# Kernel optimization log

Measured on AMD Instinct MI355X. Metric: run time of the kernel, lower is better.

## Reference

```python
import jax, jax.numpy as jnp
import numpy as np

N_NODES = 100000

def gcn_conv(x, edge_index, W, b):
    # PyG GCNConv: y = D^{-1/2} (A + I) D^{-1/2} X W + b
    N = x.shape[0]
    xw = x @ W  # transform first (smaller feature dim for message passing)
    loop = jnp.arange(N, dtype=edge_index.dtype)
    src = jnp.concatenate([edge_index[0], loop])
    dst = jnp.concatenate([edge_index[1], loop])
    ones = jnp.ones(dst.shape[0], dtype=xw.dtype)
    deg = jax.ops.segment_sum(ones, dst, num_segments=N)
    dinv = jnp.where(deg > 0, jax.lax.rsqrt(deg), 0.0)
    norm = dinv[src] * dinv[dst]  # [E+N]
    msg = xw[src] * norm[:, None]  # gather + scale
    out = jax.ops.segment_sum(msg, dst, num_segments=N)  # scatter-add
    return out + b

def setup_inputs() -> dict:
    key = jax.random.key(0)
    k1, k2, k3, k4, k5 = jax.random.split(key, 5)
    num_features, hidden, num_classes = 500, 64, 40
    x = jax.random.normal(k1, (N_NODES, num_features), dtype=jnp.float32)
    edge_index = jax.random.randint(k2, (2, 1600000), 0, N_NODES, dtype=jnp.int64)
    # Glorot-style init for GCNConv weights, zero bias (PyG default)
    W1 = jax.random.normal(k3, (num_features, hidden), dtype=jnp.float32) / np.sqrt(num_features)
    b1 = jnp.zeros((hidden,), dtype=jnp.float32)
    W2 = jax.random.normal(k4, (hidden, num_classes), dtype=jnp.float32) / np.sqrt(hidden)
    b2 = jnp.zeros((num_classes,), dtype=jnp.float32)
    return {"x": x, "edge_index": edge_index, "W1": W1, "b1": b1, "W2": W2, "b2": b2}

def reference(x, edge_index, W1, b1, W2, b2):
    h = gcn_conv(x, edge_index, W1, b1)
    h = jax.nn.relu(h)
    # dropout is identity in eval mode (training=False)
    logits = gcn_conv(h, edge_index, W2, b2)
    return (jax.nn.log_softmax(logits, axis=1), logits)
```

## Files before the change

kernel.cpp:

```cpp
#include <hip/hip_runtime.h>
#include <hip/hip_bf16.h>
#include <math.h>

#define N_NODES 100000
#define F_IN    500
#define HID     64
#define NCLS    40
#define NBKT    ((N_NODES + 255) / 256)
#define CAP     8192

typedef __attribute__((ext_vector_type(8))) short short8v;
typedef __attribute__((ext_vector_type(4))) float floatx4;
typedef unsigned short ushort_t;
typedef unsigned int uint_t;

__device__ __forceinline__ float bflo(uint_t u) {
    union { uint_t i; float f; } v; v.i = u << 16; return v.f;
}
__device__ __forceinline__ float bfhi(uint_t u) {
    union { uint_t i; float f; } v; v.i = u & 0xffff0000u; return v.f;
}
__device__ __forceinline__ ushort_t f2bf(float f) {
    __hip_bfloat16 b = __float2bfloat16(f);
    return *(ushort_t*)&b;
}
__device__ __forceinline__ uint_t pack2(float a, float b) {
    return (uint_t)f2bf(a) | ((uint_t)f2bf(b) << 16);
}

__global__ __launch_bounds__(256) void prep_kernel(const float* __restrict__ W1,
                                                   ushort_t* __restrict__ W1T,
                                                   int* __restrict__ bcursor) {
    if (blockIdx.x == 0) {
        bcursor[threadIdx.x]       = threadIdx.x * CAP;
        bcursor[threadIdx.x + 256] = (threadIdx.x + 256) * CAP;
    }
    int idx = blockIdx.x * 256 + threadIdx.x;
    if (idx >= HID * 512) return;
    int nn = idx >> 9;
    int k  = idx & 511;
    float v = (k < F_IN) ? W1[(size_t)k * HID + nn] : 0.0f;
    W1T[idx] = f2bf(v);
}

__global__ __launch_bounds__(512) void fill_kernel(const int* __restrict__ src,
                                                   const int* __restrict__ dst,
                                                   int* __restrict__ bcursor,
                                                   int* __restrict__ pairs, int E) {
    __shared__ int c[NBKT];
    __shared__ int base[NBKT];
    for (int i = threadIdx.x; i < NBKT; i += 512) c[i] = 0;
    __syncthreads();
    int chunk = (E + gridDim.x - 1) / gridDim.x;
    int lo = blockIdx.x * chunk;
    int hi = min(lo + chunk, E);
    for (int e = lo + threadIdx.x; e < hi; e += 512) atomicAdd(&c[dst[e] >> 8], 1);
    __syncthreads();
    for (int i = threadIdx.x; i < NBKT; i += 512) {
        int nn = c[i];
        base[i] = nn ? atomicAdd(&bcursor[i], nn) : 0;
    }
    __syncthreads();
    for (int i = threadIdx.x; i < NBKT; i += 512) c[i] = 0;
    __syncthreads();
    for (int e = lo + threadIdx.x; e < hi; e += 512) {
        int d = dst[e];
        int b = d >> 8;
        int p = base[b] + atomicAdd(&c[b], 1);
        if (p < (b + 1) * CAP) pairs[p] = src[e] | ((d & 255) << 17);
    }
}

__global__ __launch_bounds__(256) void b_fine_kernel(const int* __restrict__ pairs,
                                                     const int* __restrict__ bcursor,
                                                     int2* __restrict__ rse,
                                                     int* __restrict__ col,
                                                     float* __restrict__ dinv, int n) {
    __shared__ int w[CAP];
    __shared__ int cs[CAP];
    __shared__ int cnt[256];
    __shared__ int scn[256];
    __shared__ int cur[256];
    int b = blockIdx.x;
    int nb0 = b << 8;
    int nodes = min(256, n - nb0);
    int g0 = b * CAP;
    int size = min(bcursor[b] - g0, CAP);
    int tid = threadIdx.x;

    for (int i = tid; i < size; i += 256) w[i] = pairs[g0 + i];
    cnt[tid] = 0;
    __syncthreads();
    for (int i = tid; i < size; i += 256) atomicAdd(&cnt[w[i] >> 17], 1);
    __syncthreads();
    int v = cnt[tid];
    scn[tid] = v;
    __syncthreads();
    for (int off = 1; off < 256; off <<= 1) {
        int t = (tid >= off) ? scn[tid - off] : 0;
        __syncthreads();
        scn[tid] += t;
        __syncthreads();
    }
    int excl = scn[tid] - v;
    cur[tid] = excl;
    if (tid < nodes) {
        rse[nb0 + tid] = make_int2(g0 + excl, g0 + excl + v);
        dinv[nb0 + tid] = rsqrtf((float)(v + 1));
    }
    __syncthreads();
    for (int i = tid; i < size; i += 256) {
        int word = w[i];
        int lpos = atomicAdd(&cur[word >> 17], 1);
        cs[lpos] = word & 0x1FFFF;
    }
    __syncthreads();
    for (int i = tid; i < size; i += 256) col[g0 + i] = cs[i];
}

__global__ __launch_bounds__(256) void gemm1_mfma(const float* __restrict__ x,
                                                  const ushort_t* __restrict__ W1T,
                                                  const float* __restrict__ dinv,
                                                  ushort_t* __restrict__ xws, int n) {
    __shared__ __align__(16) ushort_t As[2][128 * 72];
    const int tid  = threadIdx.x;
    const int wave = tid >> 6;
    const int lane = tid & 63;
    const int m16  = lane & 15;
    const int q    = lane >> 4;
    const int r0   = blockIdx.x * 128;

    floatx4 acc[2][4];
#pragma unroll
    for (int i = 0; i < 2; i++)
#pragma unroll
        for (int j = 0; j < 4; j++) acc[i][j] = (floatx4){0.f, 0.f, 0.f, 0.f};

    const int kg    = tid & 15;
    const int rbase = tid >> 4;

    floatx4 pf[8];
    const floatx4 zero4 = (floatx4){0.f, 0.f, 0.f, 0.f};
    {
        const int k4 = kg * 4;
#pragma unroll
        for (int rr = 0; rr < 8; rr++) {
            int gr = r0 + rbase + rr * 16;
            pf[rr] = (gr < n) ? __builtin_nontemporal_load((const floatx4*)&x[(size_t)gr * F_IN + k4])
                              : zero4;
        }
#pragma unroll
        for (int rr = 0; rr < 8; rr++) {
            int row = rbase + rr * 16;
            *(uint2*)&As[0][row * 72 + kg * 4] =
                make_uint2(pack2(pf[rr][0], pf[rr][1]), pack2(pf[rr][2], pf[rr][3]));
        }
    }
    __syncthreads();

    for (int it = 0; it < 8; it++) {
        const int cur = it & 1;
        if (it < 7) {
            const int k4 = (it + 1) * 64 + kg * 4;
            const bool kok = (k4 < F_IN);
#pragma unroll
            for (int rr = 0; rr < 8; rr++) {
                int gr = r0 + rbase + rr * 16;
                pf[rr] = (kok && gr < n)
                           ? __builtin_nontemporal_load((const floatx4*)&x[(size_t)gr * F_IN + k4])
                           : zero4;
            }
        }
        const int kb = it * 64;
#pragma unroll
        for (int kt = 0; kt < 2; kt++) {
            const int ko = kt * 32 + q * 8;
            short8v a0 = *(const short8v*)&As[cur][(wave * 32 + m16) * 72 + ko];
            short8v a1 = *(const short8v*)&As[cur][(wave * 32 + 16 + m16) * 72 + ko];
#pragma unroll
            for (int nt = 0; nt < 4; nt++) {
                short8v b = *(const short8v*)&W1T[(size_t)(nt * 16 + m16) * 512 + kb + ko];
                acc[0][nt] = __builtin_amdgcn_mfma_f32_16x16x32_bf16(a0, b, acc[0][nt], 0, 0, 0);
                acc[1][nt] = __builtin_amdgcn_mfma_f32_16x16x32_bf16(a1, b, acc[1][nt], 0, 0, 0);
            }
        }
        if (it < 7) {
#pragma unroll
            for (int rr = 0; rr < 8; rr++) {
                int row = rbase + rr * 16;
                *(uint2*)&As[1 - cur][row * 72 + kg * 4] =
                    make_uint2(pack2(pf[rr][0], pf[rr][1]), pack2(pf[rr][2], pf[rr][3]));
            }
            __syncthreads();
        }
    }

#pragma unroll
    for (int mt = 0; mt < 2; mt++) {
#pragma unroll
        for (int i = 0; i < 4; i++) {
            int gr = r0 + wave * 32 + mt * 16 + q * 4 + i;
            if (gr < n) {
                float di = dinv[gr];
#pragma unroll
                for (int nt = 0; nt < 4; nt++) {
                    xws[(size_t)gr * HID + nt * 16 + m16] = f2bf(acc[mt][nt][i] * di);
                }
            }
        }
    }
}

__global__ __launch_bounds__(256) void agg1_kernel(const ushort_t* __restrict__ xws,
                                                   const int* __restrict__ col,
                                                   const int2* __restrict__ rse,
                                                   const float* __restrict__ dinv,
                                                   const float* __restrict__ b1,
                                                   ushort_t* __restrict__ hs, int n) {
    int d = blockIdx.x * 4 + (threadIdx.x >> 6);
    if (d >= n) return;
    int lane = threadIdx.x & 63;
    int g = lane >> 3;
    int c = lane & 7;
    int2 se = rse[d];
    int start = se.x, end = se.y;
    uint4 selfv = *(const uint4*)&xws[(size_t)d * HID + c * 8];
    float acc[8];
#pragma unroll
    for (int i = 0; i < 8; i++) acc[i] = 0.f;
    for (int j = start; j < end; j += 32) {
#pragma unroll
        for (int t = 0; t < 4; t++) {
            int e = j + t * 8 + g;
            if (e < end) {
                int s = col[e];
                uint4 v = *(const uint4*)&xws[(size_t)s * HID + c * 8];
                acc[0] += bflo(v.x); acc[1] += bfhi(v.x);
                acc[2] += bflo(v.y); acc[3] += bfhi(v.y);
                acc[4] += bflo(v.z); acc[5] += bfhi(v.z);
                acc[6] += bflo(v.w); acc[7] += bfhi(v.w);
            }
        }
    }
#pragma unroll
    for (int off = 8; off <= 32; off <<= 1) {
#pragma unroll
        for (int i = 0; i < 8; i++) acc[i] += __shfl_xor(acc[i], off);
    }
    acc[0] += bflo(selfv.x); acc[1] += bfhi(selfv.x);
    acc[2] += bflo(selfv.y); acc[3] += bfhi(selfv.y);
    acc[4] += bflo(selfv.z); acc[5] += bfhi(selfv.z);
    acc[6] += bflo(selfv.w); acc[7] += bfhi(selfv.w);
    if (g == 0) {
        float di = dinv[d];
        float4 b0 = *(const float4*)&b1[c * 8];
        float4 b4 = *(const float4*)&b1[c * 8 + 4];
        uint4 o;
        o.x = pack2(fmaxf(di * acc[0] + b0.x, 0.f) * di, fmaxf(di * acc[1] + b0.y, 0.f) * di);
        o.y = pack2(fmaxf(di * acc[2] + b0.z, 0.f) * di, fmaxf(di * acc[3] + b0.w, 0.f) * di);
        o.z = pack2(fmaxf(di * acc[4] + b4.x, 0.f) * di, fmaxf(di * acc[5] + b4.y, 0.f) * di);
        o.w = pack2(fmaxf(di * acc[6] + b4.z, 0.f) * di, fmaxf(di * acc[7] + b4.w, 0.f) * di);
        *(uint4*)&hs[(size_t)d * HID + c * 8] = o;
    }
}

__global__ __launch_bounds__(256) void agg2_lsm_kernel(const ushort_t* __restrict__ hs,
                                                       const int* __restrict__ col,
                                                       const int2* __restrict__ rse,
                                                       const float* __restrict__ dinv,
                                                       const float* __restrict__ W2,
                                                       const float* __restrict__ b2,
                                                       float* __restrict__ out, int n) {
    __shared__ float W2L[HID * 41];
    for (int i = threadIdx.x; i < HID * NCLS; i += 256) {
        int j = i / NCLS, k = i % NCLS;
        W2L[j * 41 + k] = W2[i];
    }
    __syncthreads();

    int d = blockIdx.x * 4 + (threadIdx.x >> 6);
    if (d >= n) return;
    int lane = threadIdx.x & 63;
    int g = lane >> 3;
    int c = lane & 7;
    int2 se = rse[d];
    int start = se.x, end = se.y;
    uint4 selfv = *(const uint4*)&hs[(size_t)d * HID + c * 8];
    float acc[8];
#pragma unroll
    for (int i = 0; i < 8; i++) acc[i] = 0.f;
    for (int j = start; j < end; j += 32) {
#pragma unroll
        for (int t = 0; t < 4; t++) {
            int e = j + t * 8 + g;
            if (e < end) {
                int s = col[e];
                uint4 v = *(const uint4*)&hs[(size_t)s * HID + c * 8];
                acc[0] += bflo(v.x); acc[1] += bfhi(v.x);
                acc[2] += bflo(v.y); acc[3] += bfhi(v.y);
                acc[4] += bflo(v.z); acc[5] += bfhi(v.z);
                acc[6] += bflo(v.w); acc[7] += bfhi(v.w);
            }
        }
    }
#pragma unroll
    for (int off = 8; off <= 32; off <<= 1) {
#pragma unroll
        for (int i = 0; i < 8; i++) acc[i] += __shfl_xor(acc[i], off);
    }
    acc[0] += bflo(selfv.x); acc[1] += bfhi(selfv.x);
    acc[2] += bflo(selfv.y); acc[3] += bfhi(selfv.y);
    acc[4] += bflo(selfv.z); acc[5] += bfhi(selfv.z);
    acc[6] += bflo(selfv.w); acc[7] += bfhi(selfv.w);

    float o[5];
#pragma unroll
    for (int kk = 0; kk < 5; kk++) {
        float s = 0.f;
#pragma unroll
        for (int i = 0; i < 8; i++)
            s += acc[i] * W2L[(c * 8 + i) * 41 + g * 5 + kk];
        o[kk] = s;
    }
#pragma unroll
    for (int off = 1; off < 8; off <<= 1) {
#pragma unroll
        for (int kk = 0; kk < 5; kk++) o[kk] += __shfl_xor(o[kk], off);
    }

    float di = dinv[d];
    float v[5];
#pragma unroll
    for (int kk = 0; kk < 5; kk++) v[kk] = di * o[kk] + b2[g * 5 + kk];

    float m = fmaxf(fmaxf(fmaxf(v[0], v[1]), fmaxf(v[2], v[3])), v[4]);
#pragma unroll
    for (int off = 8; off <= 32; off <<= 1) m = fmaxf(m, __shfl_xor(m, off));
    float s = __expf(v[0] - m) + __expf(v[1] - m) + __expf(v[2] - m)
            + __expf(v[3] - m) + __expf(v[4] - m);
#pragma unroll
    for (int off = 8; off <= 32; off <<= 1) s += __shfl_xor(s, off);

    if (c == 0) {
        float lg = __logf(s);
        float* lsm    = out;
        float* logits = out + (size_t)N_NODES * NCLS;
        size_t base = (size_t)d * NCLS + g * 5;
#pragma unroll
        for (int kk = 0; kk < 5; kk++) {
            logits[base + kk] = v[kk];
            lsm[base + kk]    = v[kk] - m - lg;
        }
    }
}

extern "C" void kernel_launch(void* const* d_in, const int* in_sizes, int n_in,
                              void* d_out, int out_size, void* d_ws, size_t ws_size,
                              hipStream_t stream) {
    const float* x  = (const float*)d_in[0];
    const int*   ei = (const int*)d_in[1];
    const float* W1 = (const float*)d_in[2];
    const float* b1 = (const float*)d_in[3];
    const float* W2 = (const float*)d_in[4];
    const float* b2 = (const float*)d_in[5];

    const int N = N_NODES;
    const int E = in_sizes[1] / 2;
    const int* src = ei;
    const int* dst = ei + E;

    ushort_t* xws  = (ushort_t*)d_ws;
    ushort_t* hsb  = xws + (size_t)N * HID;
    ushort_t* W1T  = hsb + (size_t)N * HID;
    float* dinv    = (float*)(W1T + (size_t)HID * 512);
    int2*  rse     = (int2*)(dinv + N);
    int*   bcursor = (int*)(rse + N);
    int*   pairs   = bcursor + 512;
    int*   col     = pairs + (size_t)NBKT * CAP;

    const int NB_W = (N + 3) / 4;

    prep_kernel<<<(HID * 512 + 255) / 256, 256, 0, stream>>>(W1, W1T, bcursor);

    fill_kernel<<<256, 512, 0, stream>>>(src, dst, bcursor, pairs, E);

    b_fine_kernel<<<NBKT, 256, 0, stream>>>(pairs, bcursor, rse, col, dinv, N);

    gemm1_mfma<<<(N + 127) / 128, 256, 0, stream>>>(x, W1T, dinv, xws, N);

    agg1_kernel<<<NB_W, 256, 0, stream>>>(xws, col, rse, dinv, b1, hsb, N);

    agg2_lsm_kernel<<<NB_W, 256, 0, stream>>>(hsb, col, rse, dinv, W2, b2, (float*)d_out, N);
}
```

Measured before the change: 500.9 us.

## Merge preprocessing kernels and overlap CSR build with first GEMM

Folds the W1 transpose into the edge-bucketing kernel as extra blocks, and runs the GEMM and the per-bucket CSR fine sort as one launch split by block index, so the two independent stages share the GPU. To remove the GEMM's dependence on dinv, the source-side normalization moves into the first aggregation, which now reads dinv per edge. The fine sort scatters directly to global col instead of staging through shared memory. This saves launches and lets graph building overlap the dense matmul, at the cost of an extra dinv gather per edge in agg1 and a memset launch.

After: 505.7 us. Within noise of the previous version (+1.0%).

```diff
diff --git a/kernel.cpp b/kernel.cpp
--- a/kernel.cpp
+++ b/kernel.cpp
@@ -8,6 +8,9 @@
 #define NCLS    40
 #define NBKT    ((N_NODES + 255) / 256)
 #define CAP     8192
+#define FILL_BLKS 512
+#define PREP_BLKS 128
+#define GEMM_BLKS ((N_NODES + 127) / 128)
 
 typedef __attribute__((ext_vector_type(8))) short short8v;
 typedef __attribute__((ext_vector_type(4))) float floatx4;
@@ -28,42 +31,37 @@
     return (uint_t)f2bf(a) | ((uint_t)f2bf(b) << 16);
 }
 
-__global__ __launch_bounds__(256) void prep_kernel(const float* __restrict__ W1,
-                                                   ushort_t* __restrict__ W1T,
-                                                   int* __restrict__ bcursor) {
-    if (blockIdx.x == 0) {
-        bcursor[threadIdx.x]       = threadIdx.x * CAP;
-        bcursor[threadIdx.x + 256] = (threadIdx.x + 256) * CAP;
-    }
-    int idx = blockIdx.x * 256 + threadIdx.x;
-    if (idx >= HID * 512) return;
-    int nn = idx >> 9;
-    int k  = idx & 511;
-    float v = (k < F_IN) ? W1[(size_t)k * HID + nn] : 0.0f;
-    W1T[idx] = f2bf(v);
-}
-
-__global__ __launch_bounds__(512) void fill_kernel(const int* __restrict__ src,
-                                                   const int* __restrict__ dst,
-                                                   int* __restrict__ bcursor,
-                                                   int* __restrict__ pairs, int E) {
+__global__ __launch_bounds__(256) void k1_fill_prep(const int* __restrict__ src,
+                                                    const int* __restrict__ dst,
+                                                    int* __restrict__ bcount,
+                                                    int* __restrict__ pairs,
+                                                    const float* __restrict__ W1,
+                                                    ushort_t* __restrict__ W1T, int E) {
+    if (blockIdx.x >= FILL_BLKS) {
+        int idx = (blockIdx.x - FILL_BLKS) * 256 + threadIdx.x;
+        int nn = idx >> 9;
+        int k  = idx & 511;
+        float v = (k < F_IN) ? W1[(size_t)k * HID + nn] : 0.0f;
+        W1T[idx] = f2bf(v);
+        return;
+    }
     __shared__ int c[NBKT];
     __shared__ int base[NBKT];
-    for (int i = threadIdx.x; i < NBKT; i += 512) c[i] = 0;
-    __syncthreads();
-    int chunk = (E + gridDim.x - 1) / gridDim.x;
+    for (int i = threadIdx.x; i < NBKT; i += 256) c[i] = 0;
+    __syncthreads();
+    int chunk = (E + FILL_BLKS - 1) / FILL_BLKS;
     int lo = blockIdx.x * chunk;
     int hi = min(lo + chunk, E);
-    for (int e = lo + threadIdx.x; e < hi; e += 512) atomicAdd(&c[dst[e] >> 8], 1);
-    __syncthreads();
-    for (int i = threadIdx.x; i < NBKT; i += 512) {
+    for (int e = lo + threadIdx.x; e < hi; e += 256) atomicAdd(&c[dst[e] >> 8], 1);
+    __syncthreads();
+    for (int i = threadIdx.x; i < NBKT; i += 256) {
         int nn = c[i];
-        base[i] = nn ? atomicAdd(&bcursor[i], nn) : 0;
-    }
-    __syncthreads();
-    for (int i = threadIdx.x; i < NBKT; i += 512) c[i] = 0;
-    __syncthreads();
-    for (int e = lo + threadIdx.x; e < hi; e += 512) {
+        base[i] = nn ? (i * CAP + atomicAdd(&bcount[i], nn)) : 0;
+    }
+    __syncthreads();
+    for (int i = threadIdx.x; i < NBKT; i += 256) c[i] = 0;
+    __syncthreads();
+    for (int e = lo + threadIdx.x; e < hi; e += 256) {
         int d = dst[e];
         int b = d >> 8;
         int p = base[b] + atomicAdd(&c[b], 1);
@@ -71,58 +69,16 @@
     }
 }
 
-__global__ __launch_bounds__(256) void b_fine_kernel(const int* __restrict__ pairs,
-                                                     const int* __restrict__ bcursor,
-                                                     int2* __restrict__ rse,
-                                                     int* __restrict__ col,
-                                                     float* __restrict__ dinv, int n) {
-    __shared__ int w[CAP];
-    __shared__ int cs[CAP];
-    __shared__ int cnt[256];
-    __shared__ int scn[256];
-    __shared__ int cur[256];
-    int b = blockIdx.x;
-    int nb0 = b << 8;
-    int nodes = min(256, n - nb0);
-    int g0 = b * CAP;
-    int size = min(bcursor[b] - g0, CAP);
-    int tid = threadIdx.x;
-
-    for (int i = tid; i < size; i += 256) w[i] = pairs[g0 + i];
-    cnt[tid] = 0;
-    __syncthreads();
-    for (int i = tid; i < size; i += 256) atomicAdd(&cnt[w[i] >> 17], 1);
-    __syncthreads();
-    int v = cnt[tid];
-    scn[tid] = v;
-    __syncthreads();
-    for (int off = 1; off < 256; off <<= 1) {
-        int t = (tid >= off) ? scn[tid - off] : 0;
-        __syncthreads();
-        scn[tid] += t;
-        __syncthreads();
-    }
-    int excl = scn[tid] - v;
-    cur[tid] = excl;
-    if (tid < nodes) {
-        rse[nb0 + tid] = make_int2(g0 + excl, g0 + excl + v);
-        dinv[nb0 + tid] = rsqrtf((float)(v + 1));
-    }
-    __syncthreads();
-    for (int i = tid; i < size; i += 256) {
-        int word = w[i];
-        int lpos = atomicAdd(&cur[word >> 17], 1);
-        cs[lpos] = word & 0x1FFFF;
-    }
-    __syncthreads();
-    for (int i = tid; i < size; i += 256) col[g0 + i] = cs[i];
-}
-
-__global__ __launch_bounds__(256) void gemm1_mfma(const float* __restrict__ x,
-                                                  const ushort_t* __restrict__ W1T,
-                                                  const float* __restrict__ dinv,
-                                                  ushort_t* __restrict__ xws, int n) {
-    __shared__ __align__(16) ushort_t As[2][128 * 72];
+union K2Shared {
+    ushort_t As[2][128 * 72];
+    struct { int w[CAP]; int cnt[256]; int scn[256]; int cur[256]; } bf;
+};
+
+__device__ __forceinline__ void gemm1_body(K2Shared& sm,
+                                           const float* __restrict__ x,
+                                           const ushort_t* __restrict__ W1T,
+                                           ushort_t* __restrict__ xws, int n) {
+    ushort_t (*As)[128 * 72] = sm.As;
     const int tid  = threadIdx.x;
     const int wave = tid >> 6;
     const int lane = tid & 63;
@@ -201,13 +157,72 @@
         for (int i = 0; i < 4; i++) {
             int gr = r0 + wave * 32 + mt * 16 + q * 4 + i;
             if (gr < n) {
-                float di = dinv[gr];
 #pragma unroll
                 for (int nt = 0; nt < 4; nt++) {
-                    xws[(size_t)gr * HID + nt * 16 + m16] = f2bf(acc[mt][nt][i] * di);
+                    xws[(size_t)gr * HID + nt * 16 + m16] = f2bf(acc[mt][nt][i]);
                 }
             }
         }
+    }
+}
+
+__device__ __forceinline__ void b_fine_body(K2Shared& sm, int b,
+                                            const int* __restrict__ pairs,
+                                            const int* __restrict__ bcount,
+                                            int2* __restrict__ rse,
+                                            int* __restrict__ col,
+                                            float* __restrict__ dinv, int n) {
+    int* w   = sm.bf.w;
+    int* cnt = sm.bf.cnt;
+    int* scn = sm.bf.scn;
+    int* cur = sm.bf.cur;
+    int nb0 = b << 8;
+    int nodes = min(256, n - nb0);
+    int g0 = b * CAP;
+    int size = min(bcount[b], CAP);
+    int tid = threadIdx.x;
+
+    for (int i = tid; i < size; i += 256) w[i] = pairs[g0 + i];
+    cnt[tid] = 0;
+    __syncthreads();
+    for (int i = tid; i < size; i += 256) atomicAdd(&cnt[w[i] >> 17], 1);
+    __syncthreads();
+    int v = cnt[tid];
+    scn[tid] = v;
+    __syncthreads();
+    for (int off = 1; off < 256; off <<= 1) {
+        int t = (tid >= off) ? scn[tid - off] : 0;
+        __syncthreads();
+        scn[tid] += t;
+        __syncthreads();
+    }
+    int excl = scn[tid] - v;
+    cur[tid] = g0 + excl;
+    if (tid < nodes) {
+        rse[nb0 + tid] = make_int2(g0 + excl, g0 + excl + v);
+        dinv[nb0 + tid] = rsqrtf((float)(v + 1));
+    }
+    __syncthreads();
+    for (int i = tid; i < size; i += 256) {
+        int word = w[i];
+        int pos = atomicAdd(&cur[word >> 17], 1);
+        col[pos] = word & 0x1FFFF;
+    }
+}
+
+__global__ __launch_bounds__(256) void k2_gemm_bfine(const float* __restrict__ x,
+                                                     const ushort_t* __restrict__ W1T,
+                                                     ushort_t* __restrict__ xws,
+                                                     const int* __restrict__ pairs,
+                                                     const int* __restrict__ bcount,
+                                                     int2* __restrict__ rse,
+                                                     int* __restrict__ col,
+                                                     float* __restrict__ dinv, int n) {
+    __shared__ __align__(16) K2Shared sm;
+    if (blockIdx.x < GEMM_BLKS) {
+        gemm1_body(sm, x, W1T, xws, n);
+    } else {
+        b_fine_body(sm, blockIdx.x - GEMM_BLKS, pairs, bcount, rse, col, dinv, n);
     }
 }
 
@@ -234,11 +249,12 @@
             int e = j + t * 8 + g;
             if (e < end) {
                 int s = col[e];
+                float ds = dinv[s];
                 uint4 v = *(const uint4*)&xws[(size_t)s * HID + c * 8];
-                acc[0] += bflo(v.x); acc[1] += bfhi(v.x);
-                acc[2] += bflo(v.y); acc[3] += bfhi(v.y);
-                acc[4] += bflo(v.z); acc[5] += bfhi(v.z);
-                acc[6] += bflo(v.w); acc[7] += bfhi(v.w);
+                acc[0] += ds * bflo(v.x); acc[1] += ds * bfhi(v.x);
+                acc[2] += ds * bflo(v.y); acc[3] += ds * bfhi(v.y);
+                acc[4] += ds * bflo(v.z); acc[5] += ds * bfhi(v.z);
+                acc[6] += ds * bflo(v.w); acc[7] += ds * bfhi(v.w);
             }
         }
     }
@@ -247,12 +263,12 @@
 #pragma unroll
         for (int i = 0; i < 8; i++) acc[i] += __shfl_xor(acc[i], off);
     }
-    acc[0] += bflo(selfv.x); acc[1] += bfhi(selfv.x);
-    acc[2] += bflo(selfv.y); acc[3] += bfhi(selfv.y);
-    acc[4] += bflo(selfv.z); acc[5] += bfhi(selfv.z);
-    acc[6] += bflo(selfv.w); acc[7] += bfhi(selfv.w);
     if (g == 0) {
         float di = dinv[d];
+        acc[0] += di * bflo(selfv.x); acc[1] += di * bfhi(selfv.x);
+        acc[2] += di * bflo(selfv.y); acc[3] += di * bfhi(selfv.y);
+        acc[4] += di * bflo(selfv.z); acc[5] += di * bfhi(selfv.z);
+        acc[6] += di * bflo(selfv.w); acc[7] += di * bfhi(selfv.w);
         float4 b0 = *(const float4*)&b1[c * 8];
         float4 b4 = *(const float4*)&b1[c * 8 + 4];
         uint4 o;
@@ -374,19 +390,17 @@
     ushort_t* W1T  = hsb + (size_t)N * HID;
     float* dinv    = (float*)(W1T + (size_t)HID * 512);
     int2*  rse     = (int2*)(dinv + N);
-    int*   bcursor = (int*)(rse + N);
-    int*   pairs   = bcursor + 512;
+    int*   bcount  = (int*)(rse + N);
+    int*   pairs   = bcount + 512;
     int*   col     = pairs + (size_t)NBKT * CAP;
 
     const int NB_W = (N + 3) / 4;
 
-    prep_kernel<<<(HID * 512 + 255) / 256, 256, 0, stream>>>(W1, W1T, bcursor);
-
-    fill_kernel<<<256, 512, 0, stream>>>(src, dst, bcursor, pairs, E);
-
-    b_fine_kernel<<<NBKT, 256, 0, stream>>>(pairs, bcursor, rse, col, dinv, N);
-
-    gemm1_mfma<<<(N + 127) / 128, 256, 0, stream>>>(x, W1T, dinv, xws, N);
+    (void)hipMemsetAsync(bcount, 0, 512 * sizeof(int), stream);
+
+    k1_fill_prep<<<FILL_BLKS + PREP_BLKS, 256, 0, stream>>>(src, dst, bcount, pairs, W1, W1T, E);
+
+    k2_gemm_bfine<<<GEMM_BLKS + NBKT, 256, 0, stream>>>(x, W1T, xws, pairs, bcount, rse, col, dinv, N);
 
     agg1_kernel<<<NB_W, 256, 0, stream>>>(xws, col, rse, dinv, b1, hsb, N);
 
```

## Transform before second aggregation via MFMA GEMM, fuse prep into fill kernel

Applied to the files above, without the earlier changes.

The second layer now multiplies h by W2 first with a new bf16 MFMA kernel, writing 48-padded class rows, so the second aggregation gathers 40-wide rows instead of 64-wide ones and no longer does a per-node matvec. Weight prep (W1 and W2 transposes) is merged into the edge-bucketing fill kernel, and the bucket cursors are zeroed with a memset instead of a prep write. b_fine scatters directly to global col instead of staging through shared memory. The cost is an extra kernel launch, an extra bf16 rounding of the logits input, and a padded intermediate buffer.

After: 473.1 us. -5.5%, faster.

```diff
diff --git a/kernel.cpp b/kernel.cpp
--- a/kernel.cpp
+++ b/kernel.cpp
@@ -6,8 +6,13 @@
 #define F_IN    500
 #define HID     64
 #define NCLS    40
+#define NZC     48
 #define NBKT    ((N_NODES + 255) / 256)
 #define CAP     8192
+#define FILL_BLKS 512
+#define PREP_ELEMS (HID * 512 + NZC * HID)
+#define PREP_BLKS (PREP_ELEMS / 256)
+#define GEMM_BLKS ((N_NODES + 127) / 128)
 
 typedef __attribute__((ext_vector_type(8))) short short8v;
 typedef __attribute__((ext_vector_type(4))) float floatx4;
@@ -28,42 +33,47 @@
     return (uint_t)f2bf(a) | ((uint_t)f2bf(b) << 16);
 }
 
-__global__ __launch_bounds__(256) void prep_kernel(const float* __restrict__ W1,
-                                                   ushort_t* __restrict__ W1T,
-                                                   int* __restrict__ bcursor) {
-    if (blockIdx.x == 0) {
-        bcursor[threadIdx.x]       = threadIdx.x * CAP;
-        bcursor[threadIdx.x + 256] = (threadIdx.x + 256) * CAP;
-    }
-    int idx = blockIdx.x * 256 + threadIdx.x;
-    if (idx >= HID * 512) return;
-    int nn = idx >> 9;
-    int k  = idx & 511;
-    float v = (k < F_IN) ? W1[(size_t)k * HID + nn] : 0.0f;
-    W1T[idx] = f2bf(v);
-}
-
-__global__ __launch_bounds__(512) void fill_kernel(const int* __restrict__ src,
-                                                   const int* __restrict__ dst,
-                                                   int* __restrict__ bcursor,
-                                                   int* __restrict__ pairs, int E) {
+__global__ __launch_bounds__(256) void k1_fill_prep(const int* __restrict__ src,
+                                                    const int* __restrict__ dst,
+                                                    int* __restrict__ bcount,
+                                                    int* __restrict__ pairs,
+                                                    const float* __restrict__ W1,
+                                                    ushort_t* __restrict__ W1T,
+                                                    const float* __restrict__ W2,
+                                                    ushort_t* __restrict__ W2bt, int E) {
+    if (blockIdx.x >= FILL_BLKS) {
+        int idx = (blockIdx.x - FILL_BLKS) * 256 + threadIdx.x;
+        if (idx < HID * 512) {
+            int nn = idx >> 9;
+            int k  = idx & 511;
+            float v = (k < F_IN) ? W1[(size_t)k * HID + nn] : 0.0f;
+            W1T[idx] = f2bf(v);
+        } else {
+            int idx2 = idx - HID * 512;
+            int nc = idx2 >> 6;
+            int k  = idx2 & 63;
+            float v = (nc < NCLS) ? W2[(size_t)k * NCLS + nc] : 0.0f;
+            W2bt[idx2] = f2bf(v);
+        }
+        return;
+    }
     __shared__ int c[NBKT];
     __shared__ int base[NBKT];
-    for (int i = threadIdx.x; i < NBKT; i += 512) c[i] = 0;
-    __syncthreads();
-    int chunk = (E + gridDim.x - 1) / gridDim.x;
+    for (int i = threadIdx.x; i < NBKT; i += 256) c[i] = 0;
+    __syncthreads();
+    int chunk = (E + FILL_BLKS - 1) / FILL_BLKS;
     int lo = blockIdx.x * chunk;
     int hi = min(lo + chunk, E);
-    for (int e = lo + threadIdx.x; e < hi; e += 512) atomicAdd(&c[dst[e] >> 8], 1);
-    __syncthreads();
-    for (int i = threadIdx.x; i < NBKT; i += 512) {
+    for (int e = lo + threadIdx.x; e < hi; e += 256) atomicAdd(&c[dst[e] >> 8], 1);
+    __syncthreads();
+    for (int i = threadIdx.x; i < NBKT; i += 256) {
         int nn = c[i];
-        base[i] = nn ? atomicAdd(&bcursor[i], nn) : 0;
-    }
-    __syncthreads();
-    for (int i = threadIdx.x; i < NBKT; i += 512) c[i] = 0;
-    __syncthreads();
-    for (int e = lo + threadIdx.x; e < hi; e += 512) {
+        base[i] = nn ? (i * CAP + atomicAdd(&bcount[i], nn)) : 0;
+    }
+    __syncthreads();
+    for (int i = threadIdx.x; i < NBKT; i += 256) c[i] = 0;
+    __syncthreads();
+    for (int e = lo + threadIdx.x; e < hi; e += 256) {
         int d = dst[e];
         int b = d >> 8;
         int p = base[b] + atomicAdd(&c[b], 1);
@@ -72,12 +82,11 @@
 }
 
 __global__ __launch_bounds__(256) void b_fine_kernel(const int* __restrict__ pairs,
-                                                     const int* __restrict__ bcursor,
+                                                     const int* __restrict__ bcount,
                                                      int2* __restrict__ rse,
                                                      int* __restrict__ col,
                                                      float* __restrict__ dinv, int n) {
     __shared__ int w[CAP];
-    __shared__ int cs[CAP];
     __shared__ int cnt[256];
     __shared__ int scn[256];
     __shared__ int cur[256];
@@ -85,7 +94,7 @@
     int nb0 = b << 8;
     int nodes = min(256, n - nb0);
     int g0 = b * CAP;
-    int size = min(bcursor[b] - g0, CAP);
+    int size = min(bcount[b], CAP);
     int tid = threadIdx.x;
 
     for (int i = tid; i < size; i += 256) w[i] = pairs[g0 + i];
@@ -103,7 +112,7 @@
         __syncthreads();
     }
     int excl = scn[tid] - v;
-    cur[tid] = excl;
+    cur[tid] = g0 + excl;
     if (tid < nodes) {
         rse[nb0 + tid] = make_int2(g0 + excl, g0 + excl + v);
         dinv[nb0 + tid] = rsqrtf((float)(v + 1));
@@ -111,11 +120,9 @@
     __syncthreads();
     for (int i = tid; i < size; i += 256) {
         int word = w[i];
-        int lpos = atomicAdd(&cur[word >> 17], 1);
-        cs[lpos] = word & 0x1FFFF;
-    }
-    __syncthreads();
-    for (int i = tid; i < size; i += 256) col[g0 + i] = cs[i];
+        int pos = atomicAdd(&cur[word >> 17], 1);
+        col[pos] = word & 0x1FFFF;
+    }
 }
 
 __global__ __launch_bounds__(256) void gemm1_mfma(const float* __restrict__ x,
@@ -247,12 +254,12 @@
 #pragma unroll
         for (int i = 0; i < 8; i++) acc[i] += __shfl_xor(acc[i], off);
     }
-    acc[0] += bflo(selfv.x); acc[1] += bfhi(selfv.x);
-    acc[2] += bflo(selfv.y); acc[3] += bfhi(selfv.y);
-    acc[4] += bflo(selfv.z); acc[5] += bfhi(selfv.z);
-    acc[6] += bflo(selfv.w); acc[7] += bfhi(selfv.w);
     if (g == 0) {
         float di = dinv[d];
+        acc[0] += bflo(selfv.x); acc[1] += bfhi(selfv.x);
+        acc[2] += bflo(selfv.y); acc[3] += bfhi(selfv.y);
+        acc[4] += bflo(selfv.z); acc[5] += bfhi(selfv.z);
+        acc[6] += bflo(selfv.w); acc[7] += bfhi(selfv.w);
         float4 b0 = *(const float4*)&b1[c * 8];
         float4 b4 = *(const float4*)&b1[c * 8 + 4];
         uint4 o;
@@ -264,20 +271,42 @@
     }
 }
 
-__global__ __launch_bounds__(256) void agg2_lsm_kernel(const ushort_t* __restrict__ hs,
+__global__ __launch_bounds__(256) void gemm2_mfma(const ushort_t* __restrict__ hs,
+                                                  const ushort_t* __restrict__ W2bt,
+                                                  ushort_t* __restrict__ zs, int n) {
+    int wave = threadIdx.x >> 6, lane = threadIdx.x & 63;
+    int m16 = lane & 15, q = lane >> 4;
+    int r0 = (blockIdx.x * 4 + wave) * 16;
+    if (r0 >= n) return;
+    floatx4 acc[3];
+#pragma unroll
+    for (int nt = 0; nt < 3; nt++) acc[nt] = (floatx4){0.f, 0.f, 0.f, 0.f};
+#pragma unroll
+    for (int kt = 0; kt < 2; kt++) {
+        short8v a = *(const short8v*)&hs[(size_t)(r0 + m16) * HID + kt * 32 + q * 8];
+#pragma unroll
+        for (int nt = 0; nt < 3; nt++) {
+            short8v b = *(const short8v*)&W2bt[(size_t)(nt * 16 + m16) * HID + kt * 32 + q * 8];
+            acc[nt] = __builtin_amdgcn_mfma_f32_16x16x32_bf16(a, b, acc[nt], 0, 0, 0);
+        }
+    }
+#pragma unroll
+    for (int i = 0; i < 4; i++) {
+        int gr = r0 + q * 4 + i;
+#pragma unroll
+        for (int nt = 0; nt < 3; nt++) {
+            int cc = nt * 16 + m16;
+            zs[(size_t)gr * NZC + cc] = (cc < NCLS) ? f2bf(acc[nt][i]) : (ushort_t)0;
+        }
+    }
+}
+
+__global__ __launch_bounds__(256) void agg2_lsm_kernel(const ushort_t* __restrict__ zs,
                                                        const int* __restrict__ col,
                                                        const int2* __restrict__ rse,
                                                        const float* __restrict__ dinv,
-                                                       const float* __restrict__ W2,
                                                        const float* __restrict__ b2,
                                                        float* __restrict__ out, int n) {
-    __shared__ float W2L[HID * 41];
-    for (int i = threadIdx.x; i < HID * NCLS; i += 256) {
-        int j = i / NCLS, k = i % NCLS;
-        W2L[j * 41 + k] = W2[i];
-    }
-    __syncthreads();
-
     int d = blockIdx.x * 4 + (threadIdx.x >> 6);
     if (d >= n) return;
     int lane = threadIdx.x & 63;
@@ -285,7 +314,9 @@
     int c = lane & 7;
     int2 se = rse[d];
     int start = se.x, end = se.y;
-    uint4 selfv = *(const uint4*)&hs[(size_t)d * HID + c * 8];
+    bool cok = (c < 6);
+    uint4 selfv = make_uint4(0, 0, 0, 0);
+    if (cok) selfv = *(const uint4*)&zs[(size_t)d * NZC + c * 8];
     float acc[8];
 #pragma unroll
     for (int i = 0; i < 8; i++) acc[i] = 0.f;
@@ -293,9 +324,9 @@
 #pragma unroll
         for (int t = 0; t < 4; t++) {
             int e = j + t * 8 + g;
-            if (e < end) {
+            if (e < end && cok) {
                 int s = col[e];
-                uint4 v = *(const uint4*)&hs[(size_t)s * HID + c * 8];
+                uint4 v = *(const uint4*)&zs[(size_t)s * NZC + c * 8];
                 acc[0] += bflo(v.x); acc[1] += bfhi(v.x);
                 acc[2] += bflo(v.y); acc[3] += bfhi(v.y);
                 acc[4] += bflo(v.z); acc[5] += bfhi(v.z);
@@ -313,44 +344,50 @@
     acc[4] += bflo(selfv.z); acc[5] += bfhi(selfv.z);
     acc[6] += bflo(selfv.w); acc[7] += bfhi(selfv.w);
 
-    float o[5];
-#pragma unroll
-    for (int kk = 0; kk < 5; kk++) {
-        float s = 0.f;
-#pragma unroll
-        for (int i = 0; i < 8; i++)
-            s += acc[i] * W2L[(c * 8 + i) * 41 + g * 5 + kk];
-        o[kk] = s;
-    }
-#pragma unroll
-    for (int off = 1; off < 8; off <<= 1) {
-#pragma unroll
-        for (int kk = 0; kk < 5; kk++) o[kk] += __shfl_xor(o[kk], off);
-    }
-
     float di = dinv[d];
-    float v[5];
-#pragma unroll
-    for (int kk = 0; kk < 5; kk++) v[kk] = di * o[kk] + b2[g * 5 + kk];
-
-    float m = fmaxf(fmaxf(fmaxf(v[0], v[1]), fmaxf(v[2], v[3])), v[4]);
-#pragma unroll
-    for (int off = 8; off <= 32; off <<= 1) m = fmaxf(m, __shfl_xor(m, off));
-    float s = __expf(v[0] - m) + __expf(v[1] - m) + __expf(v[2] - m)
-            + __expf(v[3] - m) + __expf(v[4] - m);
-#pragma unroll
-    for (int off = 8; off <= 32; off <<= 1) s += __shfl_xor(s, off);
-
-    if (c == 0) {
-        float lg = __logf(s);
+    bool act = (c < 5);
+    float4 b0 = make_float4(0.f, 0.f, 0.f, 0.f);
+    float4 b4 = make_float4(0.f, 0.f, 0.f, 0.f);
+    if (act) {
+        b0 = *(const float4*)&b2[c * 8];
+        b4 = *(const float4*)&b2[c * 8 + 4];
+    }
+    float v[8];
+    v[0] = di * acc[0] + b0.x; v[1] = di * acc[1] + b0.y;
+    v[2] = di * acc[2] + b0.z; v[3] = di * acc[3] + b0.w;
+    v[4] = di * acc[4] + b4.x; v[5] = di * acc[5] + b4.y;
+    v[6] = di * acc[6] + b4.z; v[7] = di * acc[7] + b4.w;
+
+    float m8 = -INFINITY;
+    if (act) {
+        m8 = fmaxf(fmaxf(fmaxf(v[0], v[1]), fmaxf(v[2], v[3])),
+                   fmaxf(fmaxf(v[4], v[5]), fmaxf(v[6], v[7])));
+    }
+#pragma unroll
+    for (int off = 1; off < 8; off <<= 1) m8 = fmaxf(m8, __shfl_xor(m8, off));
+    float s8 = 0.f;
+    if (act) {
+        s8 = __expf(v[0] - m8) + __expf(v[1] - m8) + __expf(v[2] - m8) + __expf(v[3] - m8)
+           + __expf(v[4] - m8) + __expf(v[5] - m8) + __expf(v[6] - m8) + __expf(v[7] - m8);
+    }
+#pragma unroll
+    for (int off = 1; off < 8; off <<= 1) s8 += __shfl_xor(s8, off);
+
+    if (act && g == 0) {
+        float lg = __logf(s8);
         float* lsm    = out;
         float* logits = out + (size_t)N_NODES * NCLS;
-        size_t base = (size_t)d * NCLS + g * 5;
-#pragma unroll
-        for (int kk = 0; kk < 5; kk++) {
-            logits[base + kk] = v[kk];
-            lsm[base + kk]    = v[kk] - m - lg;
-        }
+        float4 lo = make_float4(v[0], v[1], v[2], v[3]);
+        float4 hi = make_float4(v[4], v[5], v[6], v[7]);
+        *(float4*)&logits[(size_t)d * NCLS + c * 8]     = lo;
+        *(float4*)&logits[(size_t)d * NCLS + c * 8 + 4] = hi;
+        float4 olo, ohi;
+        olo.x = v[0] - m8 - lg; olo.y = v[1] - m8 - lg;
+        olo.z = v[2] - m8 - lg; olo.w = v[3] - m8 - lg;
+        ohi.x = v[4] - m8 - lg; ohi.y = v[5] - m8 - lg;
+        ohi.z = v[6] - m8 - lg; ohi.w = v[7] - m8 - lg;
+        *(float4*)&lsm[(size_t)d * NCLS + c * 8]     = olo;
+        *(float4*)&lsm[(size_t)d * NCLS + c * 8 + 4] = ohi;
     }
 }
 
@@ -371,24 +408,29 @@
 
     ushort_t* xws  = (ushort_t*)d_ws;
     ushort_t* hsb  = xws + (size_t)N * HID;
-    ushort_t* W1T  = hsb + (size_t)N * HID;
-    float* dinv    = (float*)(W1T + (size_t)HID * 512);
+    ushort_t* zsb  = hsb + (size_t)N * HID;
+    ushort_t* W1T  = zsb + (size_t)N * NZC;
+    ushort_t* W2bt = W1T + (size_t)HID * 512;
+    float* dinv    = (float*)(W2bt + NZC * HID);
     int2*  rse     = (int2*)(dinv + N);
-    int*   bcursor = (int*)(rse + N);
-    int*   pairs   = bcursor + 512;
+    int*   bcount  = (int*)(rse + N);
+    int*   pairs   = bcount + 512;
     int*   col     = pairs + (size_t)NBKT * CAP;
 
     const int NB_W = (N + 3) / 4;
 
-    prep_kernel<<<(HID * 512 + 255) / 256, 256, 0, stream>>>(W1, W1T, bcursor);
-
-    fill_kernel<<<256, 512, 0, stream>>>(src, dst, bcursor, pairs, E);
-
-    b_fine_kernel<<<NBKT, 256, 0, stream>>>(pairs, bcursor, rse, col, dinv, N);
-
-    gemm1_mfma<<<(N + 127) / 128, 256, 0, stream>>>(x, W1T, dinv, xws, N);
+    (void)hipMemsetAsync(bcount, 0, 512 * sizeof(int), stream);
+
+    k1_fill_prep<<<FILL_BLKS + PREP_BLKS, 256, 0, stream>>>(src, dst, bcount, pairs,
+                                                           W1, W1T, W2, W2bt, E);
+
+    b_fine_kernel<<<NBKT, 256, 0, stream>>>(pairs, bcount, rse, col, dinv, N);
+
+    gemm1_mfma<<<GEMM_BLKS, 256, 0, stream>>>(x, W1T, dinv, xws, N);
 
     agg1_kernel<<<NB_W, 256, 0, stream>>>(xws, col, rse, dinv, b1, hsb, N);
 
-    agg2_lsm_kernel<<<NB_W, 256, 0, stream>>>(hsb, col, rse, dinv, W2, b2, (float*)d_out, N);
-}
+    gemm2_mfma<<<(N / 16 + 3) / 4, 256, 0, stream>>>(hsb, W2bt, zsb, N);
+
+    agg2_lsm_kernel<<<NB_W, 256, 0, stream>>>(zsb, col, rse, dinv, b2, (float*)d_out, N);
+}
```
